# Kernel tuning notes

Measured on AMD Instinct MI355X. Metric: run time of the kernel, lower is better.

Reference implementation:

```python
import jax, jax.numpy as jnp
import numpy as np

B, H, W, F_HEX, F_GLB = 2, 48, 48, 150, 7
D, NH, L, DF, M = 512, 8, 4, 2048, 128
MAX_W, MAX_H, ATK, REC = 48, 48, 8, 20
S = H * W
DK = D // NH


def _ln(x, g, b):
    m = jnp.mean(x, -1, keepdims=True)
    v = jnp.mean(jnp.square(x - m), -1, keepdims=True)
    return (x - m) * jax.lax.rsqrt(v + 1e-5) * g + b


def _mha(q, k, v, wq, bq, wk, bk, wv, bv, wo, bo, mask=None):
    Bq, Sq, _ = q.shape
    Sk = k.shape[1]
    Q = (q @ wq + bq).reshape(Bq, Sq, NH, DK)
    K = (k @ wk + bk).reshape(Bq, Sk, NH, DK)
    V = (v @ wv + bv).reshape(Bq, Sk, NH, DK)
    s = jnp.einsum('bqhd,bkhd->bhqk', Q, K) / np.float32(np.sqrt(DK))
    if mask is not None:
        s = jnp.where(mask == 0, jnp.float32(-1e9), s)
    a = jax.nn.softmax(s, -1)
    o = jnp.einsum('bhqk,bkhd->bqhd', a, V).reshape(Bq, Sq, D)
    return o @ wo + bo


def setup_inputs():
    key = jax.random.key(0)
    ks = iter(jax.random.split(key, 64))
    w = lambda *sh: jax.random.normal(next(ks), sh, jnp.float32) * 0.02
    z = lambda *sh: jnp.zeros(sh, jnp.float32)
    o = lambda *sh: jnp.ones(sh, jnp.float32)
    return dict(
        map_representation=jax.random.normal(next(ks), (B, H, W, F_HEX), jnp.float32),
        global_features=jax.random.normal(next(ks), (B, F_GLB), jnp.float32),
        memory=jax.random.normal(next(ks), (B, M, D), jnp.float32),
        fog_mask=jax.random.randint(next(ks), (B, H, W), 0, 2, jnp.int32),
        hex_w=w(F_HEX, D), hex_b=z(D), glob_w=w(F_GLB, D), glob_b=z(D),
        mem_wq=w(D, D), mem_bq=z(D), mem_wk=w(D, D), mem_bk=z(D),
        mem_wv=w(D, D), mem_bv=z(D), mem_wo=w(D, D), mem_bo=z(D),
        gate_w=w(2 * D, D), gate_b=z(D),
        mn1_g=o(D), mn1_b=z(D), mn2_g=o(D), mn2_b=z(D),
        lw_q=w(L, D, D), lb_q=z(L, D), lw_k=w(L, D, D), lb_k=z(L, D),
        lw_v=w(L, D, D), lb_v=z(L, D), lw_o=w(L, D, D), lb_o=z(L, D),
        ln1_g=o(L, D), ln1_b=z(L, D), ln2_g=o(L, D), ln2_b=z(L, D),
        ff1_w=w(L, D, DF), ff1_b=z(L, DF), ff2_w=w(L, DF, D), ff2_b=z(L, D),
        pool_w=w(D, 1), pool_b=z(1),
        sx_w=w(D, MAX_W), sx_b=z(MAX_W), sy_w=w(D, MAX_H), sy_b=z(MAX_H),
        tx_w=w(D, MAX_W), tx_b=z(MAX_W), ty_w=w(D, MAX_H), ty_b=z(MAX_H),
        atk_w=w(D, ATK), atk_b=z(ATK), rec_w=w(D, REC), rec_b=z(REC),
        et_w=w(D, 1), et_b=z(1), val_w=w(D, 1), val_b=z(1),
    )


def reference(map_representation, global_features, memory, fog_mask,
              hex_w, hex_b, glob_w, glob_b,
              mem_wq, mem_bq, mem_wk, mem_bk, mem_wv, mem_bv, mem_wo, mem_bo,
              gate_w, gate_b, mn1_g, mn1_b, mn2_g, mn2_b,
              lw_q, lb_q, lw_k, lb_k, lw_v, lb_v, lw_o, lb_o,
              ln1_g, ln1_b, ln2_g, ln2_b, ff1_w, ff1_b, ff2_w, ff2_b,
              pool_w, pool_b, sx_w, sx_b, sy_w, sy_b, tx_w, tx_b, ty_w, ty_b,
              atk_w, atk_b, rec_w, rec_b, et_w, et_b, val_w, val_b):
    # project hex + global features, flatten map to token sequence [B,S,D]
    hexf = map_representation @ hex_w + hex_b
    glob = global_features @ glob_w + glob_b
    seq = (hexf + glob[:, None, None, :]).reshape(B, S, D)
    am = fog_mask.reshape(B, S)[:, None, None, :]  # key mask [B,1,1,S]

    # memory module: cross-attn conditioning + gated memory update (shared MHA weights)
    mem_out = _mha(seq, memory, memory, mem_wq, mem_bq, mem_wk, mem_bk, mem_wv, mem_bv, mem_wo, mem_bo)
    x = _ln(seq + mem_out, mn1_g, mn1_b)
    mem_upd = _mha(memory, seq, seq, mem_wq, mem_bq, mem_wk, mem_bk, mem_wv, mem_bv, mem_wo, mem_bo)
    gate = jax.nn.sigmoid(jnp.concatenate([memory, mem_upd], -1) @ gate_w + gate_b)
    new_memory = _ln(gate * mem_upd + (1.0 - gate) * memory, mn2_g, mn2_b)

    def block(xc, p):
        wq, bq, wk, bk, wv, bv, wo, bo, g1, b1, g2, b2, f1w, f1b, f2w, f2b = p
        att = _mha(xc, xc, xc, wq, bq, wk, bk, wv, bv, wo, bo, mask=am)
        xc = _ln(xc + att, g1, b1)
        h = jax.nn.gelu(xc @ f1w + f1b, approximate=False) @ f2w + f2b
        return _ln(xc + h, g2, b2), None

    x, _ = jax.lax.scan(block, x, (lw_q, lb_q, lw_k, lb_k, lw_v, lb_v, lw_o, lb_o,
                                   ln1_g, ln1_b, ln2_g, ln2_b, ff1_w, ff1_b, ff2_w, ff2_b))

    # attention pooling over tokens
    pw = jax.nn.softmax((x @ pool_w + pool_b)[..., 0], -1)  # [B,S]
    pooled = jnp.einsum('bs,bsd->bd', pw, x)

    return (pooled @ sx_w + sx_b, pooled @ sy_w + sy_b,
            pooled @ tx_w + tx_b, pooled @ ty_w + ty_b,
            pooled @ atk_w + atk_b, pooled @ rec_w + rec_b,
            pooled @ et_w + et_b, pooled @ val_w + val_b, new_memory)
```

## Files before the change

### kernel.cpp

```cpp
#include <hip/hip_runtime.h>
#include <hip/hip_bf16.h>

typedef __hip_bfloat16 bf16;
typedef unsigned short u16;
typedef __attribute__((ext_vector_type(8))) short short8;
typedef __attribute__((ext_vector_type(4))) float f32x4;

__device__ inline float b2f(u16 u){ unsigned int x = ((unsigned int)u) << 16; float f; __builtin_memcpy(&f, &x, 4); return f; }
__device__ inline u16 f2bits(float f){ __hip_bfloat16 h = __float2bfloat16(f); u16 u; __builtin_memcpy(&u, &h, 2); return u; }
__device__ inline void unpk(unsigned int w, float& a, float& b){ a = b2f((u16)(w & 0xffffu)); b = b2f((u16)(w >> 16)); }

__device__ __forceinline__ unsigned int pkbf(float a, float b)
{
  unsigned int ua = __float_as_uint(a) + 0x8000u;
  unsigned int ub = __float_as_uint(b) + 0x8000u;
  return __builtin_amdgcn_perm(ub, ua, 0x07060302u);
}

__global__ __launch_bounds__(512) void detect_k(const unsigned int* __restrict__ raw, int* __restrict__ flag)
{
  __shared__ int cnt;
  if (threadIdx.x == 0) cnt = 0;
  __syncthreads();
  unsigned int w = raw[threadIdx.x];
  unsigned int b = w & 0x7fffu;
  int pat = (b >= 0x2000u && b <= 0x4400u) ? 1 : 0;
#pragma unroll
  for (int o = 32; o; o >>= 1) pat += __shfl_xor(pat, o);
  if ((threadIdx.x & 63) == 0) atomicAdd(&cnt, pat);
  __syncthreads();
  if (threadIdx.x == 0) flag[0] = (cnt > 320) ? 1 : 0;
}

struct CvtArgs { const void* p[55]; int off[56]; int sz[55]; };

__global__ __launch_bounds__(256) void cvtall8_k(CvtArgs a, bf16* __restrict__ dst,
                                                 const int* __restrict__ flag)
{
  int g8 = blockIdx.x * 256 + threadIdx.x;
  int gid = g8 * 8;
  if (gid >= a.off[55]) return;
  int lo = 0, hi = 54;
  while (lo < hi) { int mid = (lo + hi + 1) >> 1; if (gid >= a.off[mid]) lo = mid; else hi = mid - 1; }
  int t = lo, i = gid - a.off[t];
  int n = a.sz[t];
  uint4 ov;
  if (flag[0]) {
    const u16* src = (const u16*)a.p[t];
    if (i + 8 <= n) {
      ov = *(const uint4*)(src + i);
    } else {
      u16 tmp[8];
#pragma unroll
      for (int j = 0; j < 8; j++) tmp[j] = (i + j < n) ? src[i + j] : (u16)0;
      __builtin_memcpy(&ov, tmp, 16);
    }
  } else {
    const float* src = (const float*)a.p[t];
    float v[8];
    if (i + 8 <= n) {
      uint4 f0 = *(const uint4*)(src + i);
      uint4 f1 = *(const uint4*)(src + i + 4);
      __builtin_memcpy(&v[0], &f0, 16);
      __builtin_memcpy(&v[4], &f1, 16);
    } else {
#pragma unroll
      for (int j = 0; j < 8; j++) v[j] = (i + j < n) ? src[i + j] : 0.f;
    }
    u16 o8[8];
#pragma unroll
    for (int j = 0; j < 8; j++) o8[j] = f2bits(v[j]);
    __builtin_memcpy(&ov, o8, 16);
  }
  *(uint4*)((u16*)dst + gid) = ov;
}

__device__ __forceinline__ float epi(float v, int mm, int nn,
                                     const bf16* bias, const bf16* res, int ldres,
                                     const float* extra, int extraDiv, float alpha, int mode)
{
  float bb = bias ? (float)bias[nn] : 0.f;
  v = v * alpha + bb;
  if (mode == 1)      v += extra[(mm / extraDiv) * 512 + nn];
  else if (mode == 2) v = 0.5f * v * (1.f + erff(v * 0.70710678118654752f));
  else if (mode == 4) v += (float)res[(size_t)mm * ldres + nn];
  else if (mode == 5) v = 1.f / (1.f + expf(-v));
  return v;
}

__global__ __launch_bounds__(256) void gemm_k(
    const bf16* __restrict__ A, int lda, long long sAb, long long sAh,
    const bf16* __restrict__ B, int ldb, long long sBb, long long sBh,
    bf16* __restrict__ C, int ldc, long long sCb, long long sCh,
    int M, int N, int K, int HZ,
    const bf16* __restrict__ bias,
    const bf16* __restrict__ res, int ldres,
    const float* __restrict__ extra, int extraDiv,
    float alpha, int mode)
{
  __shared__ u16 As[2][64][40];
  __shared__ u16 Bs[2][64][40];
  int z = blockIdx.z;
  int bz = z / HZ, hz = z - bz * HZ;
  A += (size_t)bz * sAb + (size_t)hz * sAh;
  B += (size_t)bz * sBb + (size_t)hz * sBh;
  C += (size_t)bz * sCb + (size_t)hz * sCh;

  int m0 = blockIdx.y * 64, n0 = blockIdx.x * 64;
  int t = threadIdx.x;
  int r = t >> 2, c0 = (t & 3) << 3;
  int lane = t & 63, wv = t >> 6, lr = lane & 15, lq = lane >> 4;

  f32x4 acc[4];
#pragma unroll
  for (int i = 0; i < 4; i++) acc[i] = (f32x4){0.f, 0.f, 0.f, 0.f};

  const u16* Ag = (const u16*)A;
  const u16* Bg = (const u16*)B;
  bool aok = (m0 + r < M), bok = (n0 + r < N);
  const u16* arow = Ag + (size_t)(m0 + r) * lda + c0;
  const u16* brow = Bg + (size_t)(n0 + r) * ldb + c0;

  uint4 av = {0u,0u,0u,0u}, bv = {0u,0u,0u,0u};
  if (aok) av = *(const uint4*)(arow);
  if (bok) bv = *(const uint4*)(brow);
  *(uint4*)&As[0][r][c0] = av;
  *(uint4*)&Bs[0][r][c0] = bv;
  if (32 < K) {
    if (aok) av = *(const uint4*)(arow + 32);
    if (bok) bv = *(const uint4*)(brow + 32);
  }
  __syncthreads();

  int buf = 0;
  for (int kt = 0; kt < K; kt += 32) {
    short8 af = *(const short8*)&As[buf][wv * 16 + lr][lq * 8];
    short8 bf0 = *(const short8*)&Bs[buf][lr][lq * 8];
    short8 bf1 = *(const short8*)&Bs[buf][16 + lr][lq * 8];
    short8 bf2 = *(const short8*)&Bs[buf][32 + lr][lq * 8];
    short8 bf3 = *(const short8*)&Bs[buf][48 + lr][lq * 8];
    int nk = kt + 32;
    if (nk < K) {
      *(uint4*)&As[buf ^ 1][r][c0] = av;
      *(uint4*)&Bs[buf ^ 1][r][c0] = bv;
      int nnk = kt + 64;
      if (nnk < K) {
        if (aok) av = *(const uint4*)(arow + nnk);
        if (bok) bv = *(const uint4*)(brow + nnk);
      }
    }
    acc[0] = __builtin_amdgcn_mfma_f32_16x16x32_bf16(af, bf0, acc[0], 0, 0, 0);
    acc[1] = __builtin_amdgcn_mfma_f32_16x16x32_bf16(af, bf1, acc[1], 0, 0, 0);
    acc[2] = __builtin_amdgcn_mfma_f32_16x16x32_bf16(af, bf2, acc[2], 0, 0, 0);
    acc[3] = __builtin_amdgcn_mfma_f32_16x16x32_bf16(af, bf3, acc[3], 0, 0, 0);
    __syncthreads();
    buf ^= 1;
  }

#pragma unroll
  for (int nt = 0; nt < 4; nt++) {
    int nn = n0 + nt * 16 + lr;
    if (nn >= N) continue;
#pragma unroll
    for (int rr = 0; rr < 4; rr++) {
      int mm = m0 + wv * 16 + lq * 4 + rr;
      if (mm >= M) continue;
      C[(size_t)mm * ldc + nn] =
          __float2bfloat16(epi(acc[nt][rr], mm, nn, bias, res, ldres, extra, extraDiv, alpha, mode));
    }
  }
}

__device__ __forceinline__ int swz(int row, int cg)
{
  return row * 64 + ((cg ^ (row & 3) ^ (((row >> 3) & 1) << 2)) << 3);
}

__global__ __launch_bounds__(256) void flash_k(
    const bf16* __restrict__ Qp, long long sQb, int sQr,
    const bf16* __restrict__ Kp, long long sKb, int sKr,
    const bf16* __restrict__ VTp, long long sVz,
    float* __restrict__ oAcc, long long sOb, long long sOsplit,
    float* __restrict__ lAcc, int Ml, int lSplit,
    const int* __restrict__ fog,
    int tilesPerSplit, int SkLen)
{
  __shared__ u16 Kl[64 * 64];
  __shared__ u16 Vl[64 * 64];
  __shared__ u16 fgl16[2304];

  const float SC = 0.125f * 1.44269504088896340736f;
  int z = blockIdx.y, b = z >> 3, h = z & 7;
  int qt = blockIdx.x;
  int split = blockIdx.z;
  int kt0 = split * tilesPerSplit;
  int t = threadIdx.x, lane = t & 63, w = t >> 6;
  int lr = lane & 15, lq = lane >> 4;
  int useMask = (fog != nullptr);

  const u16* Qg = (const u16*)Qp + (size_t)b * sQb + h * 64;
  const u16* Kg = (const u16*)Kp + (size_t)b * sKb + h * 64;
  const u16* Vg = (const u16*)VTp + (size_t)z * sVz;

  if (useMask) {
    for (int j = t; j < SkLen; j += 256) fgl16[j] = fog[b * 2304 + j] ? 0xFFFFu : 0u;
  }

  int qrow = qt * 64 + w * 16 + lr;
  short8 qf0, qf1;
  {
    union { short8 s; u16 u[8]; } i0, i1, o0, o1;
    i0.s = *(const short8*)(Qg + (size_t)qrow * sQr + lq * 8);
    i1.s = *(const short8*)(Qg + (size_t)qrow * sQr + 32 + lq * 8);
#pragma unroll
    for (int j = 0; j < 8; j++) {
      o0.u[j] = f2bits(b2f(i0.u[j]) * SC);
      o1.u[j] = f2bits(b2f(i1.u[j]) * SC);
    }
    qf0 = o0.s; qf1 = o1.s;
  }

  short8 ones8;
  {
    union { short8 s; u16 u[8]; } on;
#pragma unroll
    for (int j = 0; j < 8; j++) on.u[j] = 0x3F80u;
    ones8 = on.s;
  }

  int rowA[4], kAd0[4], kAd1[4];
#pragma unroll
  for (int nt = 0; nt < 4; nt++) {
    rowA[nt] = 32 * (nt >> 1) + 8 * (lr >> 2) + 4 * (nt & 1) + (lr & 3);
    kAd0[nt] = swz(rowA[nt], lq);
    kAd1[nt] = swz(rowA[nt], lq + 4);
  }
  int vAd0[4], vAd1[4];
#pragma unroll
  for (int dt = 0; dt < 4; dt++) {
    vAd0[dt] = swz(dt * 16 + lr, lq);
    vAd1[dt] = swz(dt * 16 + lr, lq + 4);
  }

  f32x4 o[4], ol;
#pragma unroll
  for (int i = 0; i < 4; i++) o[i] = (f32x4){0.f, 0.f, 0.f, 0.f};
  ol = (f32x4){0.f, 0.f, 0.f, 0.f};

  int rr = t >> 2, cg = t & 3, cs = cg * 8;
  int wAd0 = swz(rr, cg), wAd1 = swz(rr, cg + 4);

  const u16* krow = Kg + (size_t)(kt0 * 64 + rr) * sKr + cs;
  const u16* vrow = Vg + (size_t)rr * SkLen + kt0 * 64 + cs;
  uint4 ka = *(const uint4*)(krow);
  uint4 kb = *(const uint4*)(krow + 32);
  uint4 va = *(const uint4*)(vrow);
  uint4 vb = *(const uint4*)(vrow + 32);

  for (int kti = 0; kti < tilesPerSplit; kti++) {
    int kt = kt0 + kti;
    __syncthreads();
    *(uint4*)&Kl[wAd0] = ka;
    *(uint4*)&Kl[wAd1] = kb;
    *(uint4*)&Vl[wAd0] = va;
    *(uint4*)&Vl[wAd1] = vb;
    if (kti + 1 < tilesPerSplit) {
      krow += (size_t)64 * sKr;
      vrow += 64;
      ka = *(const uint4*)(krow);
      kb = *(const uint4*)(krow + 32);
      va = *(const uint4*)(vrow);
      vb = *(const uint4*)(vrow + 32);
    }
    __syncthreads();

    f32x4 s[4];
#pragma unroll
    for (int nt = 0; nt < 4; nt++) {
      s[nt] = (f32x4){0.f, 0.f, 0.f, 0.f};
      short8 kf0 = *(const short8*)&Kl[kAd0[nt]];
      short8 kf1 = *(const short8*)&Kl[kAd1[nt]];
      s[nt] = __builtin_amdgcn_mfma_f32_16x16x32_bf16(kf0, qf0, s[nt], 0, 0, 0);
      s[nt] = __builtin_amdgcn_mfma_f32_16x16x32_bf16(kf1, qf1, s[nt], 0, 0, 0);
    }

    union { unsigned int u[4]; short8 s8; } pk0, pk1;
#pragma unroll
    for (int nt = 0; nt < 4; nt++) {
      float p0 = __builtin_amdgcn_exp2f(s[nt][0]);
      float p1 = __builtin_amdgcn_exp2f(s[nt][1]);
      float p2 = __builtin_amdgcn_exp2f(s[nt][2]);
      float p3 = __builtin_amdgcn_exp2f(s[nt][3]);
      unsigned int w0 = pkbf(p0, p1);
      unsigned int w1 = pkbf(p2, p3);
      if (useMask) {
        int key = kt * 64 + 32 * (nt >> 1) + 8 * lq + 4 * (nt & 1);
        uint2 mm = *(const uint2*)&fgl16[key];
        w0 &= mm.x; w1 &= mm.y;
      }
      if (nt < 2) { pk0.u[(nt & 1) * 2] = w0; pk0.u[(nt & 1) * 2 + 1] = w1; }
      else        { pk1.u[(nt & 1) * 2] = w0; pk1.u[(nt & 1) * 2 + 1] = w1; }
    }
#pragma unroll
    for (int dt = 0; dt < 4; dt++) {
      short8 vf0 = *(const short8*)&Vl[vAd0[dt]];
      short8 vf1 = *(const short8*)&Vl[vAd1[dt]];
      o[dt] = __builtin_amdgcn_mfma_f32_16x16x32_bf16(pk0.s8, vf0, o[dt], 0, 0, 0);
      o[dt] = __builtin_amdgcn_mfma_f32_16x16x32_bf16(pk1.s8, vf1, o[dt], 0, 0, 0);
    }
    ol = __builtin_amdgcn_mfma_f32_16x16x32_bf16(pk0.s8, ones8, ol, 0, 0, 0);
    ol = __builtin_amdgcn_mfma_f32_16x16x32_bf16(pk1.s8, ones8, ol, 0, 0, 0);
  }

  float* lS = lAcc + (size_t)split * lSplit;
  if (lr == 0) {
#pragma unroll
    for (int r2 = 0; r2 < 4; r2++)
      lS[z * Ml + qt * 64 + w * 16 + lq * 4 + r2] = ol[r2];
  }

  float* ob = oAcc + (size_t)split * sOsplit + (size_t)b * sOb;
  int qb = qt * 64 + w * 16 + lq * 4;
#pragma unroll
  for (int dt = 0; dt < 4; dt++)
#pragma unroll
    for (int r2 = 0; r2 < 4; r2++)
      ob[(size_t)(qb + r2) * 512 + h * 64 + dt * 16 + lr] = o[dt][r2];
}

__global__ __launch_bounds__(256) void fdiv4_k(const float* __restrict__ oAcc,
                                               const float* __restrict__ lAcc,
                                               int Mq, int Ml, int rows,
                                               bf16* __restrict__ out,
                                               int nsplit, long long oSplit, int lSplit)
{
  int i = (blockIdx.x * 256 + threadIdx.x) * 4;
  if (i >= rows * 512) return;
  int row = i >> 9, col = i & 511;
  int b = row / Mq, q = row - b * Mq;
  int zz = b * 8 + (col >> 6);
  float l = 0.f;
  float4 v = {0.f, 0.f, 0.f, 0.f};
  for (int s = 0; s < nsplit; s++) {
    l += lAcc[(size_t)s * lSplit + zz * Ml + q];
    float4 p = *(const float4*)(oAcc + (size_t)s * oSplit + i);
    v.x += p.x; v.y += p.y; v.z += p.z; v.w += p.w;
  }
  float inv = (l > 0.f) ? 1.f / l : 0.f;
  u16 o4[4] = {f2bits(v.x * inv), f2bits(v.y * inv), f2bits(v.z * inv), f2bits(v.w * inv)};
  unsigned int lo = o4[0] | ((unsigned)o4[1] << 16);
  unsigned int hi = o4[2] | ((unsigned)o4[3] << 16);
  *(uint2*)((u16*)out + i) = (uint2){lo, hi};
}

__global__ void biasfuse_k(const bf16* __restrict__ mbq, const bf16* __restrict__ mbk,
                           const bf16* __restrict__ mbv, const bf16* __restrict__ lbq,
                           const bf16* __restrict__ lbk, const bf16* __restrict__ lbv,
                           bf16* __restrict__ out)
{
  int j = blockIdx.x * 256 + threadIdx.x;
  if (j >= 5 * 1536) return;
  int g = j / 1536, r = j - g * 1536;
  int which = r >> 9, c = r & 511;
  const bf16* src;
  if (g == 0) src = (which == 0) ? mbq : (which == 1) ? mbk : mbv;
  else {
    const bf16* base = (which == 0) ? lbq : (which == 1) ? lbk : lbv;
    src = base + (g - 1) * 512;
  }
  out[j] = src[c];
}

__global__ __launch_bounds__(256) void transpose_k(const bf16* __restrict__ in, bf16* __restrict__ out,
                                                   int R, int C, int Rpad, long long inB, long long outB)
{
  __shared__ u16 tile[32][33];
  const u16* ip = (const u16*)in + (size_t)blockIdx.z * inB;
  u16* op = (u16*)out + (size_t)blockIdx.z * outB;
  int c0 = blockIdx.x * 32, r0 = blockIdx.y * 32;
  int tx = threadIdx.x & 31, ty = threadIdx.x >> 5;
#pragma unroll
  for (int j = 0; j < 4; j++) {
    int rr = r0 + ty + j * 8, cc = c0 + tx;
    u16 v = 0;
    if (rr < R && cc < C) v = ip[(size_t)rr * C + cc];
    tile[ty + j * 8][tx] = v;
  }
  __syncthreads();
#pragma unroll
  for (int j = 0; j < 4; j++) {
    int oc = c0 + ty + j * 8;
    if (oc < C && r0 + tx < Rpad) op[(size_t)oc * Rpad + r0 + tx] = tile[tx][ty + j * 8];
  }
}

__global__ __launch_bounds__(256) void headT_k(const bf16* __restrict__ in, bf16* __restrict__ out,
                                               int Sk, int rowbase, int bstride, int instride)
{
  __shared__ u16 tile[32][33];
  int z = blockIdx.z, b = z >> 3, h = z & 7;
  const u16* ip = (const u16*)in + ((size_t)(rowbase + b * bstride)) * instride + h * 64;
  u16* op = (u16*)out + (size_t)z * 64 * Sk;
  int r0 = blockIdx.x * 32, c0 = blockIdx.y * 32;
  int tx = threadIdx.x & 31, ty = threadIdx.x >> 5;
#pragma unroll
  for (int j = 0; j < 4; j++)
    tile[ty + j * 8][tx] = ip[(size_t)(r0 + ty + j * 8) * instride + c0 + tx];
  __syncthreads();
#pragma unroll
  for (int j = 0; j < 4; j++)
    op[(size_t)(c0 + ty + j * 8) * Sk + r0 + tx] = tile[tx][ty + j * 8];
}

__global__ __launch_bounds__(256) void ln_k(const bf16* __restrict__ in, const bf16* __restrict__ g,
                                            const bf16* __restrict__ bb, bf16* __restrict__ out)
{
  size_t row = blockIdx.x * 4 + (threadIdx.x >> 6);
  int lane = threadIdx.x & 63;
  const u16* ip = (const u16*)in + row * 512 + lane * 8;
  uint4 rv = *(const uint4*)ip;
  float v[8];
  unpk(rv.x, v[0], v[1]); unpk(rv.y, v[2], v[3]); unpk(rv.z, v[4], v[5]); unpk(rv.w, v[6], v[7]);
  float s = 0.f, s2 = 0.f;
#pragma unroll
  for (int k = 0; k < 8; k++) { s += v[k]; s2 += v[k] * v[k]; }
#pragma unroll
  for (int o = 32; o; o >>= 1) { s += __shfl_xor(s, o); s2 += __shfl_xor(s2, o); }
  float mean = s * (1.f / 512.f);
  float var = s2 * (1.f / 512.f) - mean * mean;
  float rstd = rsqrtf(var + 1e-5f);
  uint4 gv = *(const uint4*)((const u16*)g + lane * 8);
  uint4 bv = *(const uint4*)((const u16*)bb + lane * 8);
  float gf[8], bf2[8];
  unpk(gv.x, gf[0], gf[1]); unpk(gv.y, gf[2], gf[3]); unpk(gv.z, gf[4], gf[5]); unpk(gv.w, gf[6], gf[7]);
  unpk(bv.x, bf2[0], bf2[1]); unpk(bv.y, bf2[2], bf2[3]); unpk(bv.z, bf2[4], bf2[5]); unpk(bv.w, bf2[6], bf2[7]);
  u16 o8[8];
#pragma unroll
  for (int k = 0; k < 8; k++) o8[k] = f2bits((v[k] - mean) * rstd * gf[k] + bf2[k]);
  uint4 ov;
  ov.x = o8[0] | ((unsigned)o8[1] << 16); ov.y = o8[2] | ((unsigned)o8[3] << 16);
  ov.z = o8[4] | ((unsigned)o8[5] << 16); ov.w = o8[6] | ((unsigned)o8[7] << 16);
  *(uint4*)((u16*)out + row * 512 + lane * 8) = ov;
}

__global__ void glob_k(const bf16* __restrict__ gf, const bf16* __restrict__ gw,
                       const bf16* __restrict__ gb, float* __restrict__ out)
{
  int i = blockIdx.x * 256 + threadIdx.x; if (i >= 1024) return;
  int b = i >> 9, d = i & 511;
  float s = (float)gb[d];
#pragma unroll
  for (int f = 0; f < 7; f++) s += (float)gf[b * 7 + f] * (float)gw[f * 512 + d];
  out[i] = s;
}

__global__ void padA_k(const bf16* __restrict__ in, bf16* __restrict__ out)
{
  int i = blockIdx.x * 256 + threadIdx.x; if (i >= 4608 * 160) return;
  int r = i / 160, c = i - r * 160;
  out[i] = (c < 150) ? in[r * 150 + c] : __float2bfloat16(0.f);
}

__global__ void catg_k(const bf16* __restrict__ mem, const bf16* __restrict__ mu, bf16* __restrict__ out)
{
  int i = blockIdx.x * 256 + threadIdx.x; if (i >= 256 * 1024) return;
  int r = i >> 10, c = i & 1023;
  out[i] = (c < 512) ? mem[r * 512 + c] : mu[r * 512 + c - 512];
}

__global__ void gcomb_k(const bf16* __restrict__ g, const bf16* __restrict__ mu,
                        const bf16* __restrict__ mem, bf16* __restrict__ out)
{
  int i = blockIdx.x * 256 + threadIdx.x; if (i >= 131072) return;
  float gg = (float)g[i];
  out[i] = __float2bfloat16(gg * (float)mu[i] + (1.f - gg) * (float)mem[i]);
}

__global__ __launch_bounds__(64) void plog_k(const bf16* __restrict__ x, const bf16* __restrict__ pw,
                                             const bf16* __restrict__ pb, float* __restrict__ out)
{
  size_t row = blockIdx.x; int lane = threadIdx.x;
  uint4 xv = *(const uint4*)((const u16*)x + row * 512 + lane * 8);
  uint4 wv = *(const uint4*)((const u16*)pw + lane * 8);
  float v[8], w[8];
  unpk(xv.x, v[0], v[1]); unpk(xv.y, v[2], v[3]); unpk(xv.z, v[4], v[5]); unpk(xv.w, v[6], v[7]);
  unpk(wv.x, w[0], w[1]); unpk(wv.y, w[2], w[3]); unpk(wv.z, w[4], w[5]); unpk(wv.w, w[6], w[7]);
  float s = 0.f;
#pragma unroll
  for (int k = 0; k < 8; k++) s += v[k] * w[k];
#pragma unroll
  for (int o = 32; o; o >>= 1) s += __shfl_xor(s, o);
  if (lane == 0) out[row] = s + (float)pb[0];
}

__global__ __launch_bounds__(256) void psm_k(const float* __restrict__ lg, float* __restrict__ pw)
{
  __shared__ float red[4];
  int b = blockIdx.x, tid = threadIdx.x;
  const float* p = lg + b * 2304;
  float vals[9]; float mx = -3e38f;
#pragma unroll
  for (int i = 0; i < 9; i++) {
    int j = tid + i * 256;
    float x = (j < 2304) ? p[j] : -3e38f;
    vals[i] = x; mx = fmaxf(mx, x);
  }
#pragma unroll
  for (int o = 32; o; o >>= 1) mx = fmaxf(mx, __shfl_xor(mx, o));
  if ((tid & 63) == 0) red[tid >> 6] = mx;
  __syncthreads();
  mx = fmaxf(fmaxf(red[0], red[1]), fmaxf(red[2], red[3]));
  float sum = 0.f;
#pragma unroll
  for (int i = 0; i < 9; i++) {
    int j = tid + i * 256;
    if (j < 2304) { float e = expf(vals[i] - mx); vals[i] = e; sum += e; }
  }
  __syncthreads();
#pragma unroll
  for (int o = 32; o; o >>= 1) sum += __shfl_xor(sum, o);
  if ((tid & 63) == 0) red[tid >> 6] = sum;
  __syncthreads();
  sum = red[0] + red[1] + red[2] + red[3];
  float inv = 1.f / sum;
#pragma unroll
  for (int i = 0; i < 9; i++) {
    int j = tid + i * 256;
    if (j < 2304) pw[b * 2304 + j] = vals[i] * inv;
  }
}

__global__ __launch_bounds__(256) void pool1_k(const float* __restrict__ pw, const bf16* __restrict__ x,
                                               float* __restrict__ out)
{
  int b = blockIdx.y, chunk = blockIdx.x, t = threadIdx.x;
  float a0 = 0.f, a1 = 0.f;
  for (int s = 0; s < 64; s++) {
    int tok = chunk * 64 + s;
    float wv = pw[b * 2304 + tok];
    const u16* xp = (const u16*)x + ((size_t)(b * 2304 + tok)) * 512;
    a0 += wv * b2f(xp[t]);
    a1 += wv * b2f(xp[t + 256]);
  }
  atomicAdd(&out[b * 512 + t], a0);
  atomicAdd(&out[b * 512 + t + 256], a1);
}

__global__ void heads_k(const float* __restrict__ pooled,
                        const bf16* w0, const bf16* b0, const bf16* w1, const bf16* b1,
                        const bf16* w2, const bf16* b2, const bf16* w3, const bf16* b3,
                        const bf16* w4, const bf16* b4, const bf16* w5, const bf16* b5,
                        const bf16* w6, const bf16* b6, const bf16* w7, const bf16* b7,
                        void* __restrict__ outv, const int* __restrict__ flag)
{
  int idx = blockIdx.x * 256 + threadIdx.x; if (idx >= 444) return;
  const bf16* W[8] = {w0, w1, w2, w3, w4, w5, w6, w7};
  const bf16* Bi[8] = {b0, b1, b2, b3, b4, b5, b6, b7};
  int b = idx / 222, j = idx - b * 222;
  const int sizes[8]  = {48, 48, 48, 48, 8, 20, 1, 1};
  const int outoff[8] = {0, 96, 192, 288, 384, 400, 440, 442};
  int h = 0, basec = 0;
  while (h < 7 && j >= basec + sizes[h]) { basec += sizes[h]; ++h; }
  int col = j - basec;
  const bf16* wp = W[h]; int nc = sizes[h];
  float s = (float)Bi[h][col];
  for (int k = 0; k < 512; k++) s += pooled[b * 512 + k] * (float)wp[k * nc + col];
  int e = outoff[h] + b * nc + col;
  if (flag[0]) ((bf16*)outv)[e] = __float2bfloat16(s);
  else         ((float*)outv)[e] = s;
}

__global__ void outstore_k(const bf16* __restrict__ nm, void* __restrict__ outv,
                           const int* __restrict__ flag)
{
  int i = blockIdx.x * 256 + threadIdx.x; if (i >= 131072) return;
  if (flag[0]) ((bf16*)outv)[444 + i] = nm[i];
  else         ((float*)outv)[444 + i] = (float)nm[i];
}


static inline void gemm(hipStream_t st, const bf16* A, int lda, long long sAb, long long sAh,
                        const bf16* B, int ldb, long long sBb, long long sBh,
                        bf16* C, int ldc, long long sCb, long long sCh,
                        int M, int N, int K, int BZ, int HZ,
                        const bf16* bias, const bf16* res, int ldres,
                        const float* extra, int extraDiv, float alpha, int mode)
{
  dim3 g((N + 63) / 64, (M + 63) / 64, BZ * HZ);
  gemm_k<<<g, dim3(256), 0, st>>>(A, lda, sAb, sAh, B, ldb, sBb, sBh, C, ldc, sCb, sCh,
                                  M, N, K, HZ, bias, res, ldres, extra, extraDiv, alpha, mode);
}

static inline void transp(hipStream_t st, const bf16* in, bf16* out, int R, int C, int Rpad,
                          long long inB, long long outB, int Z)
{
  dim3 g((C + 31) / 32, (Rpad + 31) / 32, Z);
  transpose_k<<<g, dim3(256), 0, st>>>(in, out, R, C, Rpad, inB, outB);
}

extern "C" void kernel_launch(void* const* d_in, const int* in_sizes, int n_in,
                              void* d_out, int out_size, void* d_ws, size_t ws_size,
                              hipStream_t stream)
{
  (void)in_sizes; (void)n_in; (void)out_size;
  const int* fog = (const int*)d_in[3];

  static const int kSz[55] = {
    691200, 14, 131072, 76800, 512, 3584, 512,
    262144, 512, 262144, 512, 262144, 512, 262144, 512,
    524288, 512, 512, 512, 512, 512,
    1048576, 2048, 1048576, 2048, 1048576, 2048, 1048576, 2048,
    2048, 2048, 2048, 2048,
    4194304, 8192, 4194304, 2048,
    512, 1,
    24576, 48, 24576, 48, 24576, 48, 24576, 48,
    4096, 8, 10240, 20, 512, 1, 512, 1};
  static const int kIdx[55] = {
    0, 1, 2, 4, 5, 6, 7,
    8, 9, 10, 11, 12, 13, 14, 15,
    16, 17, 18, 19, 20, 21,
    22, 23, 24, 25, 26, 27, 28, 29,
    30, 31, 32, 33,
    34, 35, 36, 37,
    38, 39,
    40, 41, 42, 43, 44, 45, 46, 47,
    48, 49, 50, 51, 52, 53, 54, 55};

  CvtArgs ca;
  size_t cum[55]; int coffi = 0;
  for (int t = 0; t < 55; t++) {
    cum[t] = (size_t)coffi;
    ca.p[t] = d_in[kIdx[t]];
    ca.off[t] = coffi;
    ca.sz[t] = kSz[t];
    coffi += (kSz[t] + 7) & ~7;
  }
  ca.off[55] = coffi;
  size_t coff = (size_t)coffi;

  const int S = 2304, NROW = 4608, CATROW = 4864;
  const long long QR = 1536;
  const long long RSQ = (long long)S * QR;
  const long long OSPLIT = (long long)NROW * 512;

  char* basep = (char*)d_ws; size_t off = 0;
  auto alloc = [&](size_t elems, size_t esz) -> void* {
    void* p = basep + off; off += (elems * esz + 255) & ~(size_t)255; return p;
  };

  bf16* canon = (bf16*)alloc(coff, 2);
  int* dflag = (int*)alloc(64, 4);
  bf16* tHex = (bf16*)alloc(512 * 160, 2);
  bf16* aPad = (bf16*)alloc((size_t)NROW * 160, 2);
  bf16* tQKVmem = (bf16*)alloc(1536 * 512, 2);
  bf16* tWo = (bf16*)alloc(512 * 512, 2);
  bf16* tGate = (bf16*)alloc(512 * 1024, 2);
  bf16* tLqkv = (bf16*)alloc(4ULL * 1536 * 512, 2);
  bf16* tLo = (bf16*)alloc(4 * 512 * 512, 2);
  bf16* tF1 = (bf16*)alloc(4ULL * 2048 * 512, 2);
  bf16* tF2 = (bf16*)alloc(4ULL * 512 * 2048, 2);
  bf16* fbias = (bf16*)alloc(5 * 1536, 2);
  float* globF = (float*)alloc(1024, 4);
  bf16* catX = (bf16*)alloc((size_t)CATROW * 512, 2);
  bf16* QKV = (bf16*)alloc((size_t)CATROW * 1536, 2);
  bf16* VmemT = (bf16*)alloc(16ULL * 64 * 128, 2);
  bf16* VsT = (bf16*)alloc(16ULL * 64 * S, 2);
  bf16* mo = (bf16*)alloc((size_t)NROW * 512, 2);
  bf16* tmp1 = (bf16*)alloc((size_t)NROW * 512, 2);
  bf16* xbuf = (bf16*)alloc((size_t)NROW * 512, 2);
  bf16* x2buf = (bf16*)alloc((size_t)NROW * 512, 2);
  bf16* mu0 = (bf16*)alloc(256 * 512, 2);
  bf16* mup = (bf16*)alloc(256 * 512, 2);
  bf16* catg = (bf16*)alloc(256 * 1024, 2);
  bf16* gateb = (bf16*)alloc(256 * 512, 2);
  bf16* nmpre = (bf16*)alloc(256 * 512, 2);
  bf16* nmout = (bf16*)alloc(256 * 512, 2);
  float* plog = (float*)alloc(NROW, 4);
  float* pwv = (float*)alloc(NROW, 4);
  float* pooledF = (float*)alloc(1024, 4);
  float* oAcc = (float*)alloc(3ULL * NROW * 512, 4);
  float* lAcc = (float*)alloc(131072, 4);
  bf16* hbuf = (bf16*)alloc((size_t)NROW * 2048, 2);
  if (off > ws_size) return;

  detect_k<<<1, 512, 0, stream>>>((const unsigned int*)d_in[0], dflag);
  cvtall8_k<<<(coffi / 8 + 255) / 256, 256, 0, stream>>>(ca, canon, dflag);

  auto T = [&](int t) -> const bf16* { return canon + cum[t]; };
  const bf16* map_rep = T(0);
  const bf16* gfeat   = T(1);
  const bf16* memin   = T(2);
  const bf16* hex_w = T(3);  const bf16* hex_b = T(4);
  const bf16* glob_w = T(5); const bf16* glob_b = T(6);
  const bf16* mem_wq = T(7);  const bf16* mem_bq = T(8);
  const bf16* mem_wk = T(9);  const bf16* mem_bk = T(10);
  const bf16* mem_wv = T(11); const bf16* mem_bv = T(12);
  const bf16* mem_wo = T(13); const bf16* mem_bo = T(14);
  const bf16* gate_w = T(15); const bf16* gate_b = T(16);
  const bf16* mn1_g = T(17); const bf16* mn1_b = T(18);
  const bf16* mn2_g = T(19); const bf16* mn2_b = T(20);
  const bf16* lw_q = T(21); const bf16* lb_q = T(22);
  const bf16* lw_k = T(23); const bf16* lb_k = T(24);
  const bf16* lw_v = T(25); const bf16* lb_v = T(26);
  const bf16* lw_o = T(27); const bf16* lb_o = T(28);
  const bf16* ln1_g = T(29); const bf16* ln1_b = T(30);
  const bf16* ln2_g = T(31); const bf16* ln2_b = T(32);
  const bf16* ff1_w = T(33); const bf16* ff1_b = T(34);
  const bf16* ff2_w = T(35); const bf16* ff2_b = T(36);
  const bf16* pool_w = T(37); const bf16* pool_b = T(38);

  transp(stream, hex_w, tHex, 150, 512, 160, 0, 0, 1);
  transp(stream, mem_wq, tQKVmem, 512, 512, 512, 0, 0, 1);
  transp(stream, mem_wk, tQKVmem + 262144, 512, 512, 512, 0, 0, 1);
  transp(stream, mem_wv, tQKVmem + 524288, 512, 512, 512, 0, 0, 1);
  transp(stream, mem_wo, tWo, 512, 512, 512, 0, 0, 1);
  transp(stream, gate_w, tGate, 1024, 512, 1024, 0, 0, 1);
  transp(stream, lw_q, tLqkv, 512, 512, 512, 262144, 786432, 4);
  transp(stream, lw_k, tLqkv + 262144, 512, 512, 512, 262144, 786432, 4);
  transp(stream, lw_v, tLqkv + 524288, 512, 512, 512, 262144, 786432, 4);
  transp(stream, lw_o, tLo, 512, 512, 512, 262144, 262144, 4);
  transp(stream, ff1_w, tF1, 512, 2048, 512, 1048576, 1048576, 4);
  transp(stream, ff2_w, tF2, 2048, 512, 2048, 1048576, 1048576, 4);
  biasfuse_k<<<(5 * 1536 + 255) / 256, 256, 0, stream>>>(mem_bq, mem_bk, mem_bv,
                                                         lb_q, lb_k, lb_v, fbias);

  glob_k<<<4, 256, 0, stream>>>(gfeat, glob_w, glob_b, globF);
  padA_k<<<(NROW * 160 + 255) / 256, 256, 0, stream>>>(map_rep, aPad);
  gemm(stream, aPad, 160, 0, 0, tHex, 160, 0, 0, catX, 512, 0, 0,
       NROW, 512, 160, 1, 1, hex_b, nullptr, 0, globF, S, 1.f, 1);
  hipMemcpyAsync(catX + (size_t)NROW * 512, memin, 256 * 512 * 2, hipMemcpyDeviceToDevice, stream);

  gemm(stream, catX, 512, 0, 0, tQKVmem, 512, 0, 0, QKV, 1536, 0, 0,
       CATROW, 1536, 512, 1, 1, fbias, nullptr, 0, nullptr, 1, 1.f, 0);

  headT_k<<<dim3(4, 2, 16), 256, 0, stream>>>(QKV + 1024, VmemT, 128, NROW, 128, 1536);
  flash_k<<<dim3(36, 16, 1), 256, 0, stream>>>(
      QKV, RSQ, 1536, QKV + (size_t)NROW * 1536 + 512, 128 * QR, 1536,
      VmemT, 64 * 128, oAcc, (long long)S * 512, OSPLIT, lAcc, 2304, 16 * 2304,
      nullptr, 2, 128);
  fdiv4_k<<<(NROW * 128 + 255) / 256, 256, 0, stream>>>(oAcc, lAcc, 2304, 2304, NROW, mo,
                                                        1, OSPLIT, 16 * 2304);
  gemm(stream, mo, 512, 0, 0, tWo, 512, 0, 0, tmp1, 512, 0, 0,
       NROW, 512, 512, 1, 1, mem_bo, catX, 512, nullptr, 1, 1.f, 4);
  ln_k<<<NROW / 4, 256, 0, stream>>>(tmp1, mn1_g, mn1_b, xbuf);

  headT_k<<<dim3(72, 2, 16), 256, 0, stream>>>(QKV + 1024, VsT, S, 0, S, 1536);
  flash_k<<<dim3(2, 16, 6), 256, 0, stream>>>(
      QKV + (size_t)NROW * 1536, 128 * QR, 1536, QKV + 512, RSQ, 1536,
      VsT, 64LL * S, oAcc, 128 * 512, 128 * 512 * 16LL, lAcc, 128, 16 * 128,
      nullptr, 6, S);
  fdiv4_k<<<(256 * 128 + 255) / 256, 256, 0, stream>>>(oAcc, lAcc, 128, 128, 256, mu0,
                                                       6, 128 * 512 * 16LL, 16 * 128);
  gemm(stream, mu0, 512, 0, 0, tWo, 512, 0, 0, mup, 512, 0, 0,
       256, 512, 512, 1, 1, mem_bo, nullptr, 0, nullptr, 1, 1.f, 0);
  catg_k<<<(256 * 1024 + 255) / 256, 256, 0, stream>>>(memin, mup, catg);
  gemm(stream, catg, 1024, 0, 0, tGate, 1024, 0, 0, gateb, 512, 0, 0,
       256, 512, 1024, 1, 1, gate_b, nullptr, 0, nullptr, 1, 1.f, 5);
  gcomb_k<<<(131072 + 255) / 256, 256, 0, stream>>>(gateb, mup, memin, nmpre);
  ln_k<<<64, 256, 0, stream>>>(nmpre, mn2_g, mn2_b, nmout);
  outstore_k<<<(131072 + 255) / 256, 256, 0, stream>>>(nmout, d_out, dflag);

  for (int l = 0; l < 4; l++) {
    gemm(stream, xbuf, 512, 0, 0, tLqkv + (size_t)l * 786432, 512, 0, 0, QKV, 1536, 0, 0,
         NROW, 1536, 512, 1, 1, fbias + (1 + l) * 1536, nullptr, 0, nullptr, 1, 1.f, 0);
    headT_k<<<dim3(72, 2, 16), 256, 0, stream>>>(QKV + 1024, VsT, S, 0, S, 1536);
    flash_k<<<dim3(36, 16, 3), 256, 0, stream>>>(
        QKV, RSQ, 1536, QKV + 512, RSQ, 1536,
        VsT, 64LL * S, oAcc, (long long)S * 512, OSPLIT, lAcc, 2304, 16 * 2304,
        fog, 12, S);
    fdiv4_k<<<(NROW * 128 + 255) / 256, 256, 0, stream>>>(oAcc, lAcc, 2304, 2304, NROW, mo,
                                                          3, OSPLIT, 16 * 2304);
    gemm(stream, mo, 512, 0, 0, tLo + (size_t)l * 262144, 512, 0, 0, tmp1, 512, 0, 0,
         NROW, 512, 512, 1, 1, lb_o + l * 512, xbuf, 512, nullptr, 1, 1.f, 4);
    ln_k<<<NROW / 4, 256, 0, stream>>>(tmp1, ln1_g + l * 512, ln1_b + l * 512, x2buf);
    gemm(stream, x2buf, 512, 0, 0, tF1 + (size_t)l * 1048576, 512, 0, 0, hbuf, 2048, 0, 0,
         NROW, 2048, 512, 1, 1, ff1_b + l * 2048, nullptr, 0, nullptr, 1, 1.f, 2);
    gemm(stream, hbuf, 2048, 0, 0, tF2 + (size_t)l * 1048576, 2048, 0, 0, tmp1, 512, 0, 0,
         NROW, 512, 2048, 1, 1, ff2_b + l * 512, x2buf, 512, nullptr, 1, 1.f, 4);
    ln_k<<<NROW / 4, 256, 0, stream>>>(tmp1, ln2_g + l * 512, ln2_b + l * 512, xbuf);
  }

  plog_k<<<NROW, 64, 0, stream>>>(xbuf, pool_w, pool_b, plog);
  psm_k<<<2, 256, 0, stream>>>(plog, pwv);
  hipMemsetAsync(pooledF, 0, 1024 * sizeof(float), stream);
  pool1_k<<<dim3(36, 2), 256, 0, stream>>>(pwv, xbuf, pooledF);

  heads_k<<<2, 256, 0, stream>>>(pooledF,
      T(39), T(40), T(41), T(42), T(43), T(44), T(45), T(46),
      T(47), T(48), T(49), T(50), T(51), T(52), T(53), T(54),
      d_out, dflag);
}
```

Measured before the change: 1.094 ms.

## Double-buffer K/V tiles in LDS for flash attention kernel

Splits the K and V shared-memory tiles into two buffers, so the next tile is written to the alternate buffer while the current one is consumed. This drops from two barriers per iteration to one. It doubles K/V LDS use, which may lower occupancy, and it moves the store of the next tile into the middle of the compute path.

```diff
diff --git a/kernel.cpp b/kernel.cpp
--- a/kernel.cpp
+++ b/kernel.cpp
@@ -185,8 +185,8 @@
     const int* __restrict__ fog,
     int tilesPerSplit, int SkLen)
 {
-  __shared__ u16 Kl[64 * 64];
-  __shared__ u16 Vl[64 * 64];
+  __shared__ u16 Kl[2][4096];
+  __shared__ u16 Vl[2][4096];
   __shared__ u16 fgl16[2304];
 
   const float SC = 0.125f * 1.44269504088896340736f;
@@ -256,32 +256,47 @@
   uint4 kb = *(const uint4*)(krow + 32);
   uint4 va = *(const uint4*)(vrow);
   uint4 vb = *(const uint4*)(vrow + 32);
-
+  *(uint4*)&Kl[0][wAd0] = ka;
+  *(uint4*)&Kl[0][wAd1] = kb;
+  *(uint4*)&Vl[0][wAd0] = va;
+  *(uint4*)&Vl[0][wAd1] = vb;
+  if (tilesPerSplit > 1) {
+    krow += (size_t)64 * sKr;
+    vrow += 64;
+    ka = *(const uint4*)(krow);
+    kb = *(const uint4*)(krow + 32);
+    va = *(const uint4*)(vrow);
+    vb = *(const uint4*)(vrow + 32);
+  }
+  __syncthreads();
+
+  int buf = 0;
   for (int kti = 0; kti < tilesPerSplit; kti++) {
     int kt = kt0 + kti;
-    __syncthreads();
-    *(uint4*)&Kl[wAd0] = ka;
-    *(uint4*)&Kl[wAd1] = kb;
-    *(uint4*)&Vl[wAd0] = va;
-    *(uint4*)&Vl[wAd1] = vb;
-    if (kti + 1 < tilesPerSplit) {
-      krow += (size_t)64 * sKr;
-      vrow += 64;
-      ka = *(const uint4*)(krow);
-      kb = *(const uint4*)(krow + 32);
-      va = *(const uint4*)(vrow);
-      vb = *(const uint4*)(vrow + 32);
-    }
-    __syncthreads();
 
     f32x4 s[4];
 #pragma unroll
     for (int nt = 0; nt < 4; nt++) {
       s[nt] = (f32x4){0.f, 0.f, 0.f, 0.f};
-      short8 kf0 = *(const short8*)&Kl[kAd0[nt]];
-      short8 kf1 = *(const short8*)&Kl[kAd1[nt]];
+      short8 kf0 = *(const short8*)&Kl[buf][kAd0[nt]];
+      short8 kf1 = *(const short8*)&Kl[buf][kAd1[nt]];
       s[nt] = __builtin_amdgcn_mfma_f32_16x16x32_bf16(kf0, qf0, s[nt], 0, 0, 0);
       s[nt] = __builtin_amdgcn_mfma_f32_16x16x32_bf16(kf1, qf1, s[nt], 0, 0, 0);
+    }
+
+    if (kti + 1 < tilesPerSplit) {
+      *(uint4*)&Kl[buf ^ 1][wAd0] = ka;
+      *(uint4*)&Kl[buf ^ 1][wAd1] = kb;
+      *(uint4*)&Vl[buf ^ 1][wAd0] = va;
+      *(uint4*)&Vl[buf ^ 1][wAd1] = vb;
+      if (kti + 2 < tilesPerSplit) {
+        krow += (size_t)64 * sKr;
+        vrow += 64;
+        ka = *(const uint4*)(krow);
+        kb = *(const uint4*)(krow + 32);
+        va = *(const uint4*)(vrow);
+        vb = *(const uint4*)(vrow + 32);
+      }
     }
 
     union { unsigned int u[4]; short8 s8; } pk0, pk1;
@@ -303,13 +318,16 @@
     }
 #pragma unroll
     for (int dt = 0; dt < 4; dt++) {
-      short8 vf0 = *(const short8*)&Vl[vAd0[dt]];
-      short8 vf1 = *(const short8*)&Vl[vAd1[dt]];
+      short8 vf0 = *(const short8*)&Vl[buf][vAd0[dt]];
+      short8 vf1 = *(const short8*)&Vl[buf][vAd1[dt]];
       o[dt] = __builtin_amdgcn_mfma_f32_16x16x32_bf16(pk0.s8, vf0, o[dt], 0, 0, 0);
       o[dt] = __builtin_amdgcn_mfma_f32_16x16x32_bf16(pk1.s8, vf1, o[dt], 0, 0, 0);
     }
     ol = __builtin_amdgcn_mfma_f32_16x16x32_bf16(pk0.s8, ones8, ol, 0, 0, 0);
     ol = __builtin_amdgcn_mfma_f32_16x16x32_bf16(pk1.s8, ones8, ol, 0, 0, 0);
+
+    __syncthreads();
+    buf ^= 1;
   }
 
   float* lS = lAcc + (size_t)split * lSplit;
```

Result: no change. 1.099 ms (+0.4%).
